# Performance work log

Measured on AMD Instinct MI355X. Metric: run time of the kernel, lower is better.

The kernel has to match this reference:

```python
import jax, jax.numpy as jnp
import numpy as np

B, IN, HID, E, C = 32768, 128, 128, 32, 128


def setup_inputs() -> dict:
    key = jax.random.key(0)
    ks = jax.random.split(key, 9)
    s_in = 1.0 / np.sqrt(IN)
    s_hid = 1.0 / np.sqrt(HID)
    return {
        "x": jax.random.normal(ks[0], (B, IN), dtype=jnp.float32),
        # Router (gate.fc1); gate.fc2 is unused in forward
        "Wg": jax.random.uniform(ks[1], (IN, E), jnp.float32, -s_in, s_in),
        "bg": jax.random.uniform(ks[2], (E,), jnp.float32, -s_in, s_in),
        # Stacked expert weights: fc1 [E, IN, HID], fc2 [E, HID, HID]
        "W1": jax.random.uniform(ks[3], (E, IN, HID), jnp.float32, -s_in, s_in),
        "b1": jax.random.uniform(ks[4], (E, HID), jnp.float32, -s_in, s_in),
        "W2": jax.random.uniform(ks[5], (E, HID, HID), jnp.float32, -s_hid, s_hid),
        "b2": jax.random.uniform(ks[6], (E, HID), jnp.float32, -s_hid, s_hid),
        # Classifier [HID, C]
        "Wc": jax.random.uniform(ks[7], (HID, C), jnp.float32, -s_hid, s_hid),
        "bc": jax.random.uniform(ks[8], (C,), jnp.float32, -s_hid, s_hid),
    }


def reference(x, Wg, bg, W1, b1, W2, b2, Wc, bc):
    # Router: softmax(relu(x @ Wg + bg)) over experts
    scores = jax.nn.softmax(jax.nn.relu(x @ Wg + bg), axis=1)  # [B, E]
    # Training path: every expert processes every token
    h = jax.nn.relu(jnp.einsum("bi,eih->beh", x, W1) + b1)      # [B, E, HID]
    eo = jnp.einsum("beh,eho->beo", h, W2) + b2                  # [B, E, HID]
    out = jnp.einsum("beh,hc->bec", eo, Wc) + bc                 # [B, E, C]
    return out, scores
```

## Files before the change

kernel.cpp:

```cpp
#include <hip/hip_runtime.h>
#include <stdint.h>

#define B_TOK 32768
#define IN    128
#define HID   128
#define NE    32
#define NC    128

typedef __attribute__((ext_vector_type(8))) __bf16 bf16x8;
typedef __attribute__((ext_vector_type(4))) float  f32x4;

static __device__ __forceinline__ unsigned short f2bf(float f) {
    union { float f; uint32_t u; } v; v.f = f;
    uint32_t u = v.u;
    return (unsigned short)((u + 0x7FFFu + ((u >> 16) & 1u)) >> 16);
}

__global__ void k_convert_x(const float* __restrict__ x, unsigned short* __restrict__ xb) {
    int i = (blockIdx.x * 256 + threadIdx.x) * 4;
    float4 v = *(const float4*)(x + i);
    ushort4 o;
    o.x = f2bf(v.x); o.y = f2bf(v.y); o.z = f2bf(v.z); o.w = f2bf(v.w);
    *(ushort4*)(xb + i) = o;
}

__global__ void k_prep_w1t(const float* __restrict__ W1, unsigned short* __restrict__ W1T) {
    int idx = blockIdx.x * 256 + threadIdx.x;
    int i = idx & 127;
    int h = (idx >> 7) & 127;
    int e = idx >> 14;
    W1T[idx] = f2bf(W1[(e * 128 + i) * 128 + h]);
}

__global__ void k_prep_w2c(const float* __restrict__ W2, const float* __restrict__ Wc,
                           const float* __restrict__ b2, const float* __restrict__ bc,
                           unsigned short* __restrict__ W2cT, float* __restrict__ bc2) {
    __shared__ float row[128];
    int e = blockIdx.x >> 7, h = blockIdx.x & 127;
    int c = threadIdx.x;
    row[c] = W2[(e * 128 + h) * 128 + c];
    __syncthreads();
    float acc = 0.f;
    #pragma unroll 8
    for (int t = 0; t < 128; ++t) acc += row[t] * Wc[t * 128 + c];
    W2cT[(e * 128 + c) * 128 + h] = f2bf(acc);
    if (h == 0) {
        float a2 = bc[c];
        for (int t = 0; t < 128; ++t) a2 += b2[e * 128 + t] * Wc[t * 128 + c];
        bc2[e * 128 + c] = a2;
    }
}

__global__ __launch_bounds__(256) void k_router(const float* __restrict__ x,
        const float* __restrict__ Wg, const float* __restrict__ bg,
        float* __restrict__ scores) {
    __shared__ float Wgs[128 * 32];
    __shared__ float xs[8][128];
    int tid = threadIdx.x;
    for (int j = tid; j < 4096; j += 256) Wgs[j] = Wg[j];
    int rb = blockIdx.x * 8;
    for (int j = tid; j < 8 * 128; j += 256)
        xs[j >> 7][j & 127] = x[(rb + (j >> 7)) * 128 + (j & 127)];
    __syncthreads();
    int r = tid >> 5;
    int e = tid & 31;
    float acc = bg[e];
    #pragma unroll 8
    for (int i = 0; i < 128; ++i) acc += xs[r][i] * Wgs[i * 32 + e];
    acc = fmaxf(acc, 0.f);
    float m = acc;
    for (int off = 16; off > 0; off >>= 1) m = fmaxf(m, __shfl_xor(m, off, 32));
    float p = __expf(acc - m);
    float s = p;
    for (int off = 16; off > 0; off >>= 1) s += __shfl_xor(s, off, 32);
    scores[(size_t)(rb + r) * 32 + e] = p / s;
}

__global__ __launch_bounds__(128, 2) void k_moe(const unsigned short* __restrict__ Xb,
        const unsigned short* __restrict__ W1T, const float* __restrict__ b1,
        const unsigned short* __restrict__ W2cT, const float* __restrict__ bc2,
        float* __restrict__ out) {
    __shared__ __align__(16) unsigned short Hs[2][64 * 136];
    const int e    = blockIdx.y;
    const int tid  = threadIdx.x;
    const int wave = tid >> 6;
    const int lane = tid & 63;
    const int l15  = lane & 15;
    const int quad = lane >> 4;
    const int row0 = blockIdx.x * 128 + wave * 64;

    bf16x8 xb[4][4];
    #pragma unroll
    for (int bt = 0; bt < 4; ++bt) {
        const unsigned short* xp = Xb + (size_t)(row0 + bt * 16 + l15) * 128 + quad * 8;
        #pragma unroll
        for (int kc = 0; kc < 4; ++kc)
            xb[bt][kc] = *(const bf16x8*)(xp + kc * 32);
    }

    const unsigned short* w1p = W1T + e * (128 * 128) + l15 * 128 + quad * 8;
    const float* b1p = b1 + e * 128 + quad * 4;
    unsigned short* hsw = &Hs[wave][0];

    #pragma unroll
    for (int nt = 0; nt < 8; ++nt) {
        bf16x8 w[4];
        const unsigned short* bp = w1p + nt * 16 * 128;
        #pragma unroll
        for (int kc = 0; kc < 4; ++kc) w[kc] = *(const bf16x8*)(bp + kc * 32);
        float4 bias = *(const float4*)(b1p + nt * 16);
        f32x4 acc[4];
        #pragma unroll
        for (int bt = 0; bt < 4; ++bt) acc[bt] = (f32x4){bias.x, bias.y, bias.z, bias.w};
        #pragma unroll
        for (int kc = 0; kc < 4; ++kc) {
            #pragma unroll
            for (int bt = 0; bt < 4; ++bt)
                acc[bt] = __builtin_amdgcn_mfma_f32_16x16x32_bf16(w[kc], xb[bt][kc], acc[bt], 0, 0, 0);
        }
        #pragma unroll
        for (int bt = 0; bt < 4; ++bt) {
            ushort4 hq;
            hq.x = f2bf(fmaxf(acc[bt][0], 0.f));
            hq.y = f2bf(fmaxf(acc[bt][1], 0.f));
            hq.z = f2bf(fmaxf(acc[bt][2], 0.f));
            hq.w = f2bf(fmaxf(acc[bt][3], 0.f));
            *(ushort4*)(hsw + (bt * 16 + l15) * 136 + nt * 16 + quad * 4) = hq;
        }
    }
    __syncthreads();

    bf16x8 hb[4][4];
    #pragma unroll
    for (int bt = 0; bt < 4; ++bt) {
        const unsigned short* hp = hsw + (bt * 16 + l15) * 136 + quad * 8;
        #pragma unroll
        for (int kc = 0; kc < 4; ++kc)
            hb[bt][kc] = *(const bf16x8*)(hp + kc * 32);
    }
    __syncthreads();

    float* stage = (float*)hsw;
    const unsigned short* w2p = W2cT + e * (128 * 128) + l15 * 128 + quad * 8;
    const float* bcp = bc2 + e * 128 + quad * 4;
    const int rsel = lane >> 5;
    const int cw   = (lane & 31) * 4;

    #pragma unroll
    for (int half = 0; half < 2; ++half) {
        #pragma unroll
        for (int nt = 0; nt < 8; ++nt) {
            bf16x8 w[4];
            const unsigned short* bp = w2p + nt * 16 * 128;
            #pragma unroll
            for (int kc = 0; kc < 4; ++kc) w[kc] = *(const bf16x8*)(bp + kc * 32);
            float4 bias = *(const float4*)(bcp + nt * 16);
            f32x4 acc[2];
            acc[0] = (f32x4){bias.x, bias.y, bias.z, bias.w};
            acc[1] = acc[0];
            #pragma unroll
            for (int kc = 0; kc < 4; ++kc) {
                #pragma unroll
                for (int btl = 0; btl < 2; ++btl)
                    acc[btl] = __builtin_amdgcn_mfma_f32_16x16x32_bf16(
                        w[kc], hb[half * 2 + btl][kc], acc[btl], 0, 0, 0);
            }
            #pragma unroll
            for (int btl = 0; btl < 2; ++btl) {
                int row = btl * 16 + l15;
                int col = (nt * 16 + quad * 4) ^ ((row & 7) << 2);
                *(f32x4*)(stage + row * 128 + col) = acc[btl];
            }
        }
        #pragma unroll
        for (int j = 0; j < 16; ++j) {
            int row = j * 2 + rsel;
            int col = cw ^ ((row & 7) << 2);
            f32x4 v = *(const f32x4*)(stage + row * 128 + col);
            float* p = out + (size_t)(row0 + half * 32 + row) * (NE * NC) + e * NC + cw;
            __builtin_nontemporal_store(v, (f32x4*)p);
        }
    }
}

extern "C" void kernel_launch(void* const* d_in, const int* in_sizes, int n_in,
                              void* d_out, int out_size, void* d_ws, size_t ws_size,
                              hipStream_t stream) {
    const float* x  = (const float*)d_in[0];
    const float* Wg = (const float*)d_in[1];
    const float* bg = (const float*)d_in[2];
    const float* W1 = (const float*)d_in[3];
    const float* b1 = (const float*)d_in[4];
    const float* W2 = (const float*)d_in[5];
    const float* b2 = (const float*)d_in[6];
    const float* Wc = (const float*)d_in[7];
    const float* bc = (const float*)d_in[8];

    float* out    = (float*)d_out;
    float* scores = out + (size_t)B_TOK * NE * NC;

    unsigned short* Xb   = (unsigned short*)d_ws;
    unsigned short* W1T  = Xb + (size_t)B_TOK * IN;
    unsigned short* W2cT = W1T + NE * IN * HID;
    float*          bc2  = (float*)(W2cT + NE * HID * NC);

    hipLaunchKernelGGL(k_convert_x, dim3((B_TOK * IN) / (256 * 4)), dim3(256), 0, stream, x, Xb);
    hipLaunchKernelGGL(k_prep_w1t,  dim3((NE * IN * HID) / 256),    dim3(256), 0, stream, W1, W1T);
    hipLaunchKernelGGL(k_prep_w2c,  dim3(NE * HID),                 dim3(128), 0, stream,
                       W2, Wc, b2, bc, W2cT, bc2);
    hipLaunchKernelGGL(k_router,    dim3(B_TOK / 8),                dim3(256), 0, stream,
                       x, Wg, bg, scores);
    hipLaunchKernelGGL(k_moe,       dim3(B_TOK / 128, NE),          dim3(128), 0, stream,
                       Xb, W1T, b1, W2cT, bc2, out);
}
```

Baseline: 741.0 us.

## Loop four experts per single-wave block with double-buffered weight prefetch

Each block is now one wave covering 64 tokens and loops over four experts. The token fragments stay in registers across those experts, and the weight fragments for the next n-tile (and the next expert's first W1 tile) are loaded into double-buffered registers while the current MFMAs run. The hidden tile in LDS now uses an XOR swizzle instead of padding. The aim is to hide global weight-load latency and cut redundant X loads. In exchange, blocks are smaller with less parallelism per block, register pressure is higher, and extra syncthreads are added around the staging buffer.

```diff
diff --git a/kernel.cpp b/kernel.cpp
--- a/kernel.cpp
+++ b/kernel.cpp
@@ -76,109 +76,137 @@
     scores[(size_t)(rb + r) * 32 + e] = p / s;
 }
 
-__global__ __launch_bounds__(128, 2) void k_moe(const unsigned short* __restrict__ Xb,
+__global__ __launch_bounds__(64, 2) void k_moe(const unsigned short* __restrict__ Xb,
         const unsigned short* __restrict__ W1T, const float* __restrict__ b1,
         const unsigned short* __restrict__ W2cT, const float* __restrict__ bc2,
         float* __restrict__ out) {
-    __shared__ __align__(16) unsigned short Hs[2][64 * 136];
-    const int e    = blockIdx.y;
-    const int tid  = threadIdx.x;
-    const int wave = tid >> 6;
-    const int lane = tid & 63;
+    __shared__ __align__(16) unsigned short Hs[64 * 128];
+    const int lane = threadIdx.x;
     const int l15  = lane & 15;
     const int quad = lane >> 4;
-    const int row0 = blockIdx.x * 128 + wave * 64;
+    const int row0 = blockIdx.x * 64;
+    const int e0   = blockIdx.y * 4;
+    const int rsel = lane >> 5;
+    const int cw   = (lane & 31) * 4;
 
     bf16x8 xb[4][4];
     #pragma unroll
     for (int bt = 0; bt < 4; ++bt) {
         const unsigned short* xp = Xb + (size_t)(row0 + bt * 16 + l15) * 128 + quad * 8;
         #pragma unroll
-        for (int kc = 0; kc < 4; ++kc)
-            xb[bt][kc] = *(const bf16x8*)(xp + kc * 32);
-    }
-
-    const unsigned short* w1p = W1T + e * (128 * 128) + l15 * 128 + quad * 8;
-    const float* b1p = b1 + e * 128 + quad * 4;
-    unsigned short* hsw = &Hs[wave][0];
-
-    #pragma unroll
-    for (int nt = 0; nt < 8; ++nt) {
-        bf16x8 w[4];
-        const unsigned short* bp = w1p + nt * 16 * 128;
-        #pragma unroll
-        for (int kc = 0; kc < 4; ++kc) w[kc] = *(const bf16x8*)(bp + kc * 32);
-        float4 bias = *(const float4*)(b1p + nt * 16);
-        f32x4 acc[4];
-        #pragma unroll
-        for (int bt = 0; bt < 4; ++bt) acc[bt] = (f32x4){bias.x, bias.y, bias.z, bias.w};
-        #pragma unroll
-        for (int kc = 0; kc < 4; ++kc) {
-            #pragma unroll
-            for (int bt = 0; bt < 4; ++bt)
-                acc[bt] = __builtin_amdgcn_mfma_f32_16x16x32_bf16(w[kc], xb[bt][kc], acc[bt], 0, 0, 0);
+        for (int kc = 0; kc < 4; ++kc) xb[bt][kc] = *(const bf16x8*)(xp + kc * 32);
+    }
+
+    bf16x8 w1f[2][4], w2f[2][4];
+    {
+        const unsigned short* bp = W1T + (size_t)e0 * 16384 + l15 * 128 + quad * 8;
+        #pragma unroll
+        for (int kc = 0; kc < 4; ++kc) w1f[0][kc] = *(const bf16x8*)(bp + kc * 32);
+    }
+
+    #pragma unroll 1
+    for (int ei = 0; ei < 4; ++ei) {
+        const int e = e0 + ei;
+        const unsigned short* w1p = W1T  + (size_t)e * 16384 + l15 * 128 + quad * 8;
+        const unsigned short* w2p = W2cT + (size_t)e * 16384 + l15 * 128 + quad * 8;
+        const float* b1p = b1  + e * 128 + quad * 4;
+        const float* bcp = bc2 + e * 128 + quad * 4;
+        const unsigned short* w1n = W1T + (size_t)(ei < 3 ? e + 1 : e) * 16384
+                                        + l15 * 128 + quad * 8;
+
+        #pragma unroll
+        for (int nt = 0; nt < 8; ++nt) {
+            const int cur = nt & 1, nxt = cur ^ 1;
+            if (nt < 7) {
+                const unsigned short* bp = w1p + (nt + 1) * 16 * 128;
+                #pragma unroll
+                for (int kc = 0; kc < 4; ++kc) w1f[nxt][kc] = *(const bf16x8*)(bp + kc * 32);
+            } else {
+                #pragma unroll
+                for (int kc = 0; kc < 4; ++kc) w2f[0][kc] = *(const bf16x8*)(w2p + kc * 32);
+            }
+            float4 bias = *(const float4*)(b1p + nt * 16);
+            f32x4 acc[4];
+            #pragma unroll
+            for (int bt = 0; bt < 4; ++bt) acc[bt] = (f32x4){bias.x, bias.y, bias.z, bias.w};
+            #pragma unroll
+            for (int kc = 0; kc < 4; ++kc) {
+                #pragma unroll
+                for (int bt = 0; bt < 4; ++bt)
+                    acc[bt] = __builtin_amdgcn_mfma_f32_16x16x32_bf16(w1f[cur][kc], xb[bt][kc], acc[bt], 0, 0, 0);
+            }
+            #pragma unroll
+            for (int bt = 0; bt < 4; ++bt) {
+                ushort4 hq;
+                hq.x = f2bf(fmaxf(acc[bt][0], 0.f));
+                hq.y = f2bf(fmaxf(acc[bt][1], 0.f));
+                hq.z = f2bf(fmaxf(acc[bt][2], 0.f));
+                hq.w = f2bf(fmaxf(acc[bt][3], 0.f));
+                int row = bt * 16 + l15;
+                int col = (nt * 16 + quad * 4) ^ ((row & 7) << 3);
+                *(ushort4*)(Hs + row * 128 + col) = hq;
+            }
         }
+        __syncthreads();
+
+        bf16x8 hb[4][4];
         #pragma unroll
         for (int bt = 0; bt < 4; ++bt) {
-            ushort4 hq;
-            hq.x = f2bf(fmaxf(acc[bt][0], 0.f));
-            hq.y = f2bf(fmaxf(acc[bt][1], 0.f));
-            hq.z = f2bf(fmaxf(acc[bt][2], 0.f));
-            hq.w = f2bf(fmaxf(acc[bt][3], 0.f));
-            *(ushort4*)(hsw + (bt * 16 + l15) * 136 + nt * 16 + quad * 4) = hq;
+            int row = bt * 16 + l15;
+            #pragma unroll
+            for (int kc = 0; kc < 4; ++kc) {
+                int col = (kc * 32 + quad * 8) ^ ((row & 7) << 3);
+                hb[bt][kc] = *(const bf16x8*)(Hs + row * 128 + col);
+            }
         }
-    }
-    __syncthreads();
-
-    bf16x8 hb[4][4];
-    #pragma unroll
-    for (int bt = 0; bt < 4; ++bt) {
-        const unsigned short* hp = hsw + (bt * 16 + l15) * 136 + quad * 8;
-        #pragma unroll
-        for (int kc = 0; kc < 4; ++kc)
-            hb[bt][kc] = *(const bf16x8*)(hp + kc * 32);
-    }
-    __syncthreads();
-
-    float* stage = (float*)hsw;
-    const unsigned short* w2p = W2cT + e * (128 * 128) + l15 * 128 + quad * 8;
-    const float* bcp = bc2 + e * 128 + quad * 4;
-    const int rsel = lane >> 5;
-    const int cw   = (lane & 31) * 4;
-
-    #pragma unroll
-    for (int half = 0; half < 2; ++half) {
-        #pragma unroll
-        for (int nt = 0; nt < 8; ++nt) {
-            bf16x8 w[4];
-            const unsigned short* bp = w2p + nt * 16 * 128;
-            #pragma unroll
-            for (int kc = 0; kc < 4; ++kc) w[kc] = *(const bf16x8*)(bp + kc * 32);
-            float4 bias = *(const float4*)(bcp + nt * 16);
-            f32x4 acc[2];
-            acc[0] = (f32x4){bias.x, bias.y, bias.z, bias.w};
-            acc[1] = acc[0];
-            #pragma unroll
-            for (int kc = 0; kc < 4; ++kc) {
-                #pragma unroll
-                for (int btl = 0; btl < 2; ++btl)
-                    acc[btl] = __builtin_amdgcn_mfma_f32_16x16x32_bf16(
-                        w[kc], hb[half * 2 + btl][kc], acc[btl], 0, 0, 0);
-            }
-            #pragma unroll
-            for (int btl = 0; btl < 2; ++btl) {
-                int row = btl * 16 + l15;
-                int col = (nt * 16 + quad * 4) ^ ((row & 7) << 2);
-                *(f32x4*)(stage + row * 128 + col) = acc[btl];
-            }
-        }
-        #pragma unroll
-        for (int j = 0; j < 16; ++j) {
-            int row = j * 2 + rsel;
-            int col = cw ^ ((row & 7) << 2);
-            f32x4 v = *(const f32x4*)(stage + row * 128 + col);
-            float* p = out + (size_t)(row0 + half * 32 + row) * (NE * NC) + e * NC + cw;
-            __builtin_nontemporal_store(v, (f32x4*)p);
+        __syncthreads();
+
+        float* stage = (float*)Hs;
+
+        #pragma unroll
+        for (int half = 0; half < 2; ++half) {
+            #pragma unroll
+            for (int nt = 0; nt < 8; ++nt) {
+                const int cur = nt & 1, nxt = cur ^ 1;
+                if (nt < 7) {
+                    const unsigned short* bp = w2p + (nt + 1) * 16 * 128;
+                    #pragma unroll
+                    for (int kc = 0; kc < 4; ++kc) w2f[nxt][kc] = *(const bf16x8*)(bp + kc * 32);
+                } else if (half == 0) {
+                    #pragma unroll
+                    for (int kc = 0; kc < 4; ++kc) w2f[nxt][kc] = *(const bf16x8*)(w2p + kc * 32);
+                } else {
+                    #pragma unroll
+                    for (int kc = 0; kc < 4; ++kc) w1f[0][kc] = *(const bf16x8*)(w1n + kc * 32);
+                }
+                float4 bias = *(const float4*)(bcp + nt * 16);
+                f32x4 acc2[2];
+                acc2[0] = (f32x4){bias.x, bias.y, bias.z, bias.w};
+                acc2[1] = acc2[0];
+                #pragma unroll
+                for (int kc = 0; kc < 4; ++kc) {
+                    #pragma unroll
+                    for (int btl = 0; btl < 2; ++btl)
+                        acc2[btl] = __builtin_amdgcn_mfma_f32_16x16x32_bf16(
+                            w2f[cur][kc], hb[half * 2 + btl][kc], acc2[btl], 0, 0, 0);
+                }
+                #pragma unroll
+                for (int btl = 0; btl < 2; ++btl) {
+                    int row = btl * 16 + l15;
+                    int col = (nt * 16 + quad * 4) ^ ((row & 7) << 2);
+                    *(f32x4*)(stage + row * 128 + col) = acc2[btl];
+                }
+            }
+            __syncthreads();
+            #pragma unroll
+            for (int j = 0; j < 16; ++j) {
+                int row = j * 2 + rsel;
+                int col = cw ^ ((row & 7) << 2);
+                f32x4 v = *(const f32x4*)(stage + row * 128 + col);
+                float* p = out + (size_t)(row0 + half * 32 + row) * (NE * NC) + e * NC + cw;
+                __builtin_nontemporal_store(v, (f32x4*)p);
+            }
+            __syncthreads();
         }
     }
 }
@@ -210,6 +238,6 @@
                        W2, Wc, b2, bc, W2cT, bc2);
     hipLaunchKernelGGL(k_router,    dim3(B_TOK / 8),                dim3(256), 0, stream,
                        x, Wg, bg, scores);
-    hipLaunchKernelGGL(k_moe,       dim3(B_TOK / 128, NE),          dim3(128), 0, stream,
+    hipLaunchKernelGGL(k_moe,       dim3(B_TOK / 64, NE / 4),       dim3(64), 0, stream,
                        Xb, W1T, b1, W2cT, bc2, out);
 }
```

Result: slower. 784.9 us (+5.9%).
